# Kernel tuning notes

Measured on AMD Instinct MI355X. Metric: run time of the kernel, lower is better.

Reference implementation:

```python
import jax, jax.numpy as jnp
import numpy as np

EPS = 1e-5

def conv2d(x, w, b, stride, pad):
    out = jax.lax.conv_general_dilated(x, w, (stride, stride), [(pad, pad), (pad, pad)],
                                       dimension_numbers=('NCHW', 'OIHW', 'NCHW'))
    return out + b[None, :, None, None]

def instance_norm(x):
    # nn.InstanceNorm2d default: affine=False, eps=1e-5, per (N,C) over (H,W)
    m = jnp.mean(x, axis=(2, 3), keepdims=True)
    v = jnp.var(x, axis=(2, 3), keepdims=True)
    return (x - m) * jax.lax.rsqrt(v + EPS)

def deform_conv2d(x, offset, mask, w, b, stride, pad):
    # x: [N,Cin,H,W]; offset: [N,2K,Ho,Wo] as [dy(K);dx(K)]; mask: [N,K,Ho,Wo]
    N, Cin, H, W = x.shape
    Cout, _, kh, kw = w.shape
    K = kh * kw
    Ho, Wo = mask.shape[2], mask.shape[3]
    oy, ox = offset[:, :K], offset[:, K:]
    ky, kx = jnp.meshgrid(jnp.arange(kh), jnp.arange(kw), indexing='ij')
    ky = ky.reshape(K).astype(x.dtype)
    kx = kx.reshape(K).astype(x.dtype)
    base_y = (jnp.arange(Ho) * stride - pad).astype(x.dtype)
    base_x = (jnp.arange(Wo) * stride - pad).astype(x.dtype)
    # sampling coords [N,K,Ho,Wo]
    py = base_y[None, None, :, None] + ky[None, :, None, None] + oy
    px = base_x[None, None, None, :] + kx[None, :, None, None] + ox
    y0 = jnp.floor(py)
    x0 = jnp.floor(px)
    wy = (py - y0)[:, None]  # [N,1,K,Ho,Wo]
    wx = (px - x0)[:, None]
    flat = x.reshape(N, Cin, H * W)

    def sample(yi, xi):
        valid = ((yi >= 0) & (yi <= H - 1) & (xi >= 0) & (xi <= W - 1)).astype(x.dtype)
        yc = jnp.clip(yi, 0, H - 1).astype(jnp.int32)
        xc = jnp.clip(xi, 0, W - 1).astype(jnp.int32)
        idx = yc * W + xc  # [N,K,Ho,Wo]
        vals = jax.vmap(lambda f, i: f[:, i])(flat, idx)  # [N,Cin,K,Ho,Wo]
        return vals * valid[:, None]

    v00 = sample(y0, x0)
    v01 = sample(y0, x0 + 1)
    v10 = sample(y0 + 1, x0)
    v11 = sample(y0 + 1, x0 + 1)
    samp = (v00 * (1 - wy) * (1 - wx) + v01 * (1 - wy) * wx
            + v10 * wy * (1 - wx) + v11 * wy * wx)
    samp = samp * mask[:, None]  # modulated (DCNv2)
    out = jnp.einsum('nckhw,ock->nohw', samp, w.reshape(Cout, Cin, K))
    return out + b[None, :, None, None]

def mdcp(x, off_w, off_b, dcn_w, dcn_b, stride, pad):
    # ModulatedDeformConvPack.forward with input_offset == input_real == x
    o = conv2d(x, off_w, off_b, stride, pad)
    K = o.shape[1] // 3
    o1, o2, m = o[:, :K], o[:, K:2 * K], o[:, 2 * K:]
    offset = jnp.concatenate([o1, o2], axis=1)
    mask = jax.nn.sigmoid(m)
    return deform_conv2d(x, offset, mask, dcn_w, dcn_b, stride, pad)

def res_block(x, w1, b1, w2, b2):
    # MUNIT-style ResBlock: [reflect-pad conv3x3, IN, ReLU] -> [reflect-pad conv3x3, IN] + skip
    h = jnp.pad(x, ((0, 0), (0, 0), (1, 1), (1, 1)), mode='reflect')
    h = jax.nn.relu(instance_norm(conv2d(h, w1, b1, 1, 0)))
    h = jnp.pad(h, ((0, 0), (0, 0), (1, 1), (1, 1)), mode='reflect')
    h = instance_norm(conv2d(h, w2, b2, 1, 0))
    return x + h

def setup_inputs() -> dict:
    key = jax.random.key(0)
    ks = jax.random.split(key, 32)
    N, H, W = 2, 256, 256

    def wconv(k, shape, scale=None):
        if scale is None:
            scale = 1.0 / np.sqrt(shape[1] * shape[2] * shape[3])
        return jax.random.normal(k, shape, jnp.float32) * scale

    def bias(k, n, scale=0.01):
        return jax.random.normal(k, (n,), jnp.float32) * scale

    inp = {}
    inp['x'] = jax.random.normal(ks[0], (N, 3, H, W), jnp.float32)
    # offset/mask convs: small weights (sub-pixel offsets; trained-from-zero in original)
    inp['off1_w'] = wconv(ks[1], (147, 3, 7, 7), 0.01)
    inp['off1_b'] = bias(ks[2], 147)
    inp['dcn1_w'] = wconv(ks[3], (64, 3, 7, 7))
    inp['dcn1_b'] = bias(ks[4], 64)
    inp['off2_w'] = wconv(ks[5], (48, 64, 4, 4), 0.01)
    inp['off2_b'] = bias(ks[6], 48)
    inp['dcn2_w'] = wconv(ks[7], (128, 64, 4, 4))
    inp['dcn2_b'] = bias(ks[8], 128)
    inp['off3_w'] = wconv(ks[9], (48, 128, 4, 4), 0.01)
    inp['off3_b'] = bias(ks[10], 48)
    inp['dcn3_w'] = wconv(ks[11], (256, 128, 4, 4))
    inp['dcn3_b'] = bias(ks[12], 256)
    for i, base in ((1, 13), (2, 17)):
        inp[f'rb{i}_w1'] = wconv(ks[base], (256, 256, 3, 3))
        inp[f'rb{i}_b1'] = bias(ks[base + 1], 256)
        inp[f'rb{i}_w2'] = wconv(ks[base + 2], (256, 256, 3, 3))
        inp[f'rb{i}_b2'] = bias(ks[base + 3], 256)
    return inp

def reference(x, off1_w, off1_b, dcn1_w, dcn1_b, off2_w, off2_b, dcn2_w, dcn2_b,
              off3_w, off3_b, dcn3_w, dcn3_b,
              rb1_w1, rb1_b1, rb1_w2, rb1_b2, rb2_w1, rb2_b1, rb2_w2, rb2_b2):
    h = jax.nn.relu(instance_norm(mdcp(x, off1_w, off1_b, dcn1_w, dcn1_b, 1, 3)))
    skip1 = h
    h = jax.nn.relu(instance_norm(mdcp(h, off2_w, off2_b, dcn2_w, dcn2_b, 2, 1)))
    skip2 = h
    h = jax.nn.relu(instance_norm(mdcp(h, off3_w, off3_b, dcn3_w, dcn3_b, 2, 1)))
    h = res_block(h, rb1_w1, rb1_b1, rb1_w2, rb1_b2)
    h = res_block(h, rb2_w1, rb2_b1, rb2_w2, rb2_b2)
    return (h, skip1, skip2)
```

## Files before the change

kernel.cpp:

```cpp
#include <hip/hip_runtime.h>
#include <hip/hip_bf16.h>
#include <math.h>

#define TPB 256
typedef __hip_bfloat16 bf16;
typedef short bf16x8 __attribute__((ext_vector_type(8)));
typedef float f32x4 __attribute__((ext_vector_type(4)));

constexpr long BIASF  = 0;
constexpr long RB1W1T = 2048;
constexpr long RB1W2T = 591872;
constexpr long RB2W1T = 1181696;
constexpr long RB2W2T = 1771520;
constexpr long FB     = 2361344;
constexpr long WB1OT  = 2361344;
constexpr long WB1DT  = 2382956;
constexpr long WO2T   = 2392364;
constexpr long WB2T   = 2441516;
constexpr long WO3T   = 2572588;
constexpr long WB3T   = 2670892;
constexpr long OFFB   = 3221504;
constexpr long H3F    = 4458496;
constexpr long PSUM   = 5507072;
constexpr long PSQ    = 5515264;
constexpr long CLBUF  = 5523456;
constexpr long OFF1B = 0,   DCN1B = 147;
constexpr long OFF2B = 211, DCN2B = 259;
constexpr long OFF3B = 387, DCN3B = 435;
constexpr long RB1B1 = 691, RB1B2 = 947;
constexpr long RB2B1 = 1203, RB2B2 = 1459;

template<int BF>
__device__ __forceinline__ float ldT(const void* p, long i) {
    if (BF) {
        unsigned short h = ((const unsigned short*)p)[i];
        return __uint_as_float(((unsigned int)h) << 16);
    }
    return ((const float*)p)[i];
}
template<int BF>
__device__ __forceinline__ void stT(void* p, long i, float v) {
    if (BF) ((bf16*)p)[i] = __float2bfloat16(v);
    else    ((float*)p)[i] = v;
}
__device__ __forceinline__ float bitsToF(unsigned short h) {
    return __uint_as_float(((unsigned int)h) << 16);
}
__device__ __forceinline__ unsigned short fToBits(float v) {
    bf16 h = __float2bfloat16(v);
    return *(unsigned short*)&h;
}

__global__ void detect_kernel(const void* __restrict__ x, int* __restrict__ flag) {
    if (threadIdx.x == 0 && blockIdx.x == 0) {
        const unsigned short* u = (const unsigned short*)x;
        int sane = 0;
        for (int i = 0; i < 256; ++i) {
            float v = bitsToF(u[i]);
            float a = fabsf(v);
            if (a > 0.0009f && a < 1100.f) ++sane;
        }
        *flag = (sane >= 224) ? 1 : 0;
    }
}

struct PtrPack { const void* p[20]; };

template<int BF>
__device__ void repack_all_body(PtrPack pp, float* __restrict__ fw)
{
    constexpr int  bcum  [11] = {0,147,211,259,387,435,691,947,1203,1459,1715};
    int j0 = blockIdx.x * 1024 + threadIdx.x * 4;
    #pragma unroll
    for (int q = 0; q < 4; ++q) {
        int j = j0 + q;
        if (j < 1715) {
            int v = 0;
            #pragma unroll
            for (int s = 1; s < 10; ++s) if (j >= bcum[s]) v = s;
            fw[BIASF + j] = ldT<BF>(pp.p[10 + v], j - bcum[v]);
        }
    }
}
__global__ __launch_bounds__(TPB) void repack_all_kernel(
    PtrPack pp, float* fw, const int* dflag) {
    if (*dflag) repack_all_body<1>(pp, fw);
    else        repack_all_body<0>(pp, fw);
}

__global__ __launch_bounds__(TPB) void repack_dcn_kernel(
    const void* __restrict__ w2, const void* __restrict__ w3,
    const void* __restrict__ w1o, const void* __restrict__ w1d,
    const void* __restrict__ w2o, const void* __restrict__ w3o,
    float* __restrict__ fw, const int* __restrict__ dflag)
{
    int bf = *dflag;
    unsigned short* wb2 = (unsigned short*)(fw + WB2T);
    unsigned short* wb3 = (unsigned short*)(fw + WB3T);
    unsigned short* wb1o = (unsigned short*)(fw + WB1OT);
    unsigned short* wb1d = (unsigned short*)(fw + WB1DT);
    unsigned short* wb2o = (unsigned short*)(fw + WO2T);
    unsigned short* wb3o = (unsigned short*)(fw + WO3T);
    int b = blockIdx.x;
    if (b < 128) {
        int e0 = b * 1024 + threadIdx.x * 4;
        #pragma unroll
        for (int j = 0; j < 4; ++j) {
            int e = e0 + j;
            int co = e >> 10, rem = e & 1023, k = rem >> 6, ci = rem & 63;
            long si = ((long)(co * 64 + ci)) * 16 + k;
            float v = bf ? ldT<1>(w2, si) : ldT<0>(w2, si);
            wb2[e] = fToBits(v);
        }
    } else if (b < 640) {
        int e0 = (b - 128) * 1024 + threadIdx.x * 4;
        #pragma unroll
        for (int j = 0; j < 4; ++j) {
            int e = e0 + j;
            int co = e >> 11, rem = e & 2047, k = rem >> 7, ci = rem & 127;
            long si = ((long)(co * 128 + ci)) * 16 + k;
            float v = bf ? ldT<1>(w3, si) : ldT<0>(w3, si);
            wb3[e] = fToBits(v);
        }
    } else if (b < 665) {
        int e0 = (b - 640) * 1024 + threadIdx.x * 4;
        #pragma unroll
        for (int j = 0; j < 4; ++j) {
            int e = e0 + j;
            int co = e / 160, k = e - co * 160;
            float v = 0.f;
            if (co < 147 && k < 147) {
                long si = (long)co * 147 + k;
                v = bf ? ldT<1>(w1o, si) : ldT<0>(w1o, si);
            }
            wb1o[e] = fToBits(v);
        }
    } else if (b < 675) {
        int e0 = (b - 665) * 1024 + threadIdx.x * 4;
        #pragma unroll
        for (int j = 0; j < 4; ++j) {
            int e = e0 + j;
            int co = e / 160, k = e - co * 160;
            float v = 0.f;
            if (k < 147) {
                long si = (long)co * 147 + k;
                v = bf ? ldT<1>(w1d, si) : ldT<0>(w1d, si);
            }
            wb1d[e] = fToBits(v);
        }
    } else if (b < 739) {
        int e0 = (b - 675) * 1024 + threadIdx.x * 4;
        #pragma unroll
        for (int j = 0; j < 4; ++j) {
            int e = e0 + j;
            int co = e >> 10, rem = e & 1023, k = rem >> 6, ci = rem & 63;
            float v = 0.f;
            if (co < 48) {
                long si = ((long)(co * 64 + ci)) * 16 + k;
                v = bf ? ldT<1>(w2o, si) : ldT<0>(w2o, si);
            }
            wb2o[e] = fToBits(v);
        }
    } else {
        int e0 = (b - 739) * 1024 + threadIdx.x * 4;
        #pragma unroll
        for (int j = 0; j < 4; ++j) {
            int e = e0 + j;
            int co = e >> 11, rem = e & 2047, k = rem >> 7, ci = rem & 127;
            float v = 0.f;
            if (co < 48) {
                long si = ((long)(co * 128 + ci)) * 16 + k;
                v = bf ? ldT<1>(w3o, si) : ldT<0>(w3o, si);
            }
            wb3o[e] = fToBits(v);
        }
    }
}

struct RbPack { const void* src[4]; };
__global__ __launch_bounds__(TPB) void repack_rb_kernel(
    RbPack rp, float* fw, const int* dflag)
{
    __shared__ unsigned short lw[4 * 2304];
    int b = blockIdx.x;
    int ten = b >> 6;
    int co0 = (b & 63) * 4;
    const void* src = rp.src[ten];
    const long dstOff[4] = {RB1W1T, RB1W2T, RB2W1T, RB2W2T};
    unsigned short* dst = (unsigned short*)(fw + dstOff[ten]);
    int bf = *dflag;
    int t = threadIdx.x;
    for (int e = t; e < 4 * 2304; e += TPB) {
        int coL = e / 2304, i = e - coL * 2304;
        long si = (long)(co0 + coL) * 2304 + i;
        float v = bf ? ldT<1>(src, si) : ldT<0>(src, si);
        lw[e] = fToBits(v);
    }
    __syncthreads();
    for (int e = t; e < 9216; e += TPB) {
        int ci = e & 255, coL = (e >> 8) & 3, q = e >> 10;
        dst[((long)q * 256 + co0 + coL) * 256 + ci] = lw[coL * 2304 + ci * 9 + q];
    }
}

template<int BF>
__device__ void layer1_mfma_body(
    const void* __restrict__ x, const unsigned short* __restrict__ wo,
    const unsigned short* __restrict__ wd, const float* __restrict__ bias1,
    const float* __restrict__ bias2, void* __restrict__ out, long obase,
    float* xs, unsigned short* A, float* offs)
{
    int b = blockIdx.x;
    int n = b >> 11;
    int ho = (b >> 3) & 255;
    int wo0 = (b & 7) << 5;
    long xn = (long)n * 3 * 65536;
    int t = threadIdx.x;

    for (int e = t; e < 3 * 7 * 40; e += TPB) {
        int cc = e % 40; int rr = (e / 40) % 7; int ci = e / 280;
        int yy = ho - 3 + rr; int xx = wo0 - 3 + cc;
        float v = 0.f;
        if (cc < 38 && yy >= 0 && yy < 256 && xx >= 0 && xx < 256)
            v = ldT<BF>(x, xn + (long)ci * 65536 + yy * 256 + xx);
        xs[e] = v;
    }
    __syncthreads();

    for (int e = t; e < 5120; e += TPB) {
        int m = e & 31, k = e >> 5;
        float v = 0.f;
        if (k < 147) {
            int ci = k / 49, q = k - ci * 49;
            int ky = q / 7, kx = q - ky * 7;
            v = xs[(ci * 7 + ky) * 40 + m + kx];
        }
        A[(k >> 5) * 1024 + m * 32 + (k & 31)] = fToBits(v);
    }
    __syncthreads();

    int wv = t >> 6, lane = t & 63;
    int quad = lane >> 4, l16 = lane & 15;
    int mt = wv & 1, ntb = wv >> 1;

    {
        f32x4 acc[5];
        #pragma unroll
        for (int j = 0; j < 5; ++j) acc[j] = (f32x4){0.f, 0.f, 0.f, 0.f};
        #pragma unroll
        for (int kc = 0; kc < 5; ++kc) {
            bf16x8 a = *(const bf16x8*)&A[(kc * 32 + mt * 16 + l16) * 32 + quad * 8];
            #pragma unroll
            for (int j = 0; j < 5; ++j) {
                int ch = (ntb + 2 * j) * 16 + l16;
                bf16x8 bw = *(const bf16x8*)&wo[ch * 160 + kc * 32 + quad * 8];
                acc[j] = __builtin_amdgcn_mfma_f32_16x16x32_bf16(a, bw, acc[j], 0, 0, 0);
            }
        }
        #pragma unroll
        for (int j = 0; j < 5; ++j) {
            int ch = (ntb + 2 * j) * 16 + l16;
            if (ch < 147) {
                float bv = bias1[ch];
                #pragma unroll
                for (int reg = 0; reg < 4; ++reg) {
                    int m = mt * 16 + quad * 4 + reg;
                    offs[ch * 34 + m] = acc[j][reg] + bv;
                }
            }
        }
    }
    __syncthreads();

    for (int e = t; e < 49 * 32; e += TPB) {
        int p = e & 31; int k = e >> 5;
        float oy = offs[k * 34 + p];
        float ox = offs[(49 + k) * 34 + p];
        float mr = offs[(98 + k) * 34 + p];
        float m = 1.f / (1.f + expf(-mr));
        float py = (float)(ho - 3 + k / 7) + oy;
        float px = (float)(wo0 + p - 3 + k % 7) + ox;
        float y0f = floorf(py), x0f = floorf(px);
        float wy = py - y0f, wx = px - x0f;
        int y0 = (int)y0f, x0 = (int)x0f;
        bool yv0 = (y0 >= 0) && (y0 < 256);
        bool yv1 = (y0 + 1 >= 0) && (y0 + 1 < 256);
        bool xv0 = (x0 >= 0) && (x0 < 256);
        bool xv1 = (x0 + 1 >= 0) && (x0 + 1 < 256);
        int y0c = min(max(y0, 0), 255), y1c = min(max(y0 + 1, 0), 255);
        int x0c = min(max(x0, 0), 255), x1c = min(max(x0 + 1, 0), 255);
        float w00 = (yv0 && xv0) ? (1.f - wy) * (1.f - wx) * m : 0.f;
        float w01 = (yv0 && xv1) ? (1.f - wy) * wx * m : 0.f;
        float w10 = (yv1 && xv0) ? wy * (1.f - wx) * m : 0.f;
        float w11 = (yv1 && xv1) ? wy * wx * m : 0.f;
        #pragma unroll
        for (int ci = 0; ci < 3; ++ci) {
            long xc = xn + (long)ci * 65536;
            float v00 = ldT<BF>(x, xc + y0c * 256 + x0c);
            float v01 = ldT<BF>(x, xc + y0c * 256 + x1c);
            float v10 = ldT<BF>(x, xc + y1c * 256 + x0c);
            float v11 = ldT<BF>(x, xc + y1c * 256 + x1c);
            float val = w00 * v00 + w01 * v01 + w10 * v10 + w11 * v11;
            int k2 = ci * 49 + k;
            A[(k2 >> 5) * 1024 + p * 32 + (k2 & 31)] = fToBits(val);
        }
    }
    __syncthreads();

    f32x4 acc2[2];
    acc2[0] = (f32x4){0.f, 0.f, 0.f, 0.f};
    acc2[1] = (f32x4){0.f, 0.f, 0.f, 0.f};
    #pragma unroll
    for (int kc = 0; kc < 5; ++kc) {
        bf16x8 a = *(const bf16x8*)&A[(kc * 32 + mt * 16 + l16) * 32 + quad * 8];
        #pragma unroll
        for (int j = 0; j < 2; ++j) {
            int co = (ntb + 2 * j) * 16 + l16;
            bf16x8 bw = *(const bf16x8*)&wd[co * 160 + kc * 32 + quad * 8];
            acc2[j] = __builtin_amdgcn_mfma_f32_16x16x32_bf16(a, bw, acc2[j], 0, 0, 0);
        }
    }
    #pragma unroll
    for (int j = 0; j < 2; ++j) {
        int co = (ntb + 2 * j) * 16 + l16;
        float bv = bias2[co];
        #pragma unroll
        for (int reg = 0; reg < 4; ++reg) {
            int wox = wo0 + mt * 16 + quad * 4 + reg;
            long oi = obase + ((long)(n * 64 + co) * 256 + ho) * 256 + wox;
            stT<BF>(out, oi, acc2[j][reg] + bv);
        }
    }
}

__global__ __launch_bounds__(TPB) void layer1_mfma_kernel(
    const void* x, const unsigned short* wo, const unsigned short* wd,
    const float* bias1, const float* bias2, void* out, long obase, const int* dflag)
{
    __shared__ __align__(16) float xs[3 * 7 * 40];
    __shared__ __align__(16) unsigned short A[5120];
    __shared__ __align__(16) float offs[147 * 34];
    if (*dflag) layer1_mfma_body<1>(x, wo, wd, bias1, bias2, out, obase, xs, A, offs);
    else        layer1_mfma_body<0>(x, wo, wd, bias1, bias2, out, obase, xs, A, offs);
}

template<int CIN, int HH, int WW, int HO, int WO>
__global__ __launch_bounds__(TPB) void offconv_mfma_kernel(
    const unsigned short* __restrict__ xcl, const unsigned short* __restrict__ wb,
    const float* __restrict__ bias_f, float* __restrict__ out)
{
    constexpr int S   = 16 * CIN;
    constexpr int KL  = 512 / CIN;
    constexpr int NCH = 16 / KL;
    constexpr int PAIRS_W = (KL * 16) / 4;
    constexpr int TILES = (HO * WO) / 16;

    __shared__ int tp[256];
    __shared__ __align__(16) unsigned short smp[16 * 512];

    int tile = blockIdx.x % TILES;
    int n    = blockIdx.x / TILES;
    int lp0  = tile * 16;

    {
        int pr = threadIdx.x;
        int k = pr >> 4, p = pr & 15;
        int lp = lp0 + p;
        int ho = lp / WO, wo = lp - ho * WO;
        int yy = ho * 2 - 1 + (k >> 2);
        int xx = wo * 2 - 1 + (k & 3);
        bool valid = (yy >= 0) && (yy < HH) && (xx >= 0) && (xx < WW);
        tp[pr] = valid ? (yy * WW + xx) * CIN : -1;
    }

    int wv = threadIdx.x >> 6, lane = threadIdx.x & 63;
    int quad = lane >> 4, l16 = lane & 15;
    const unsigned short* xn = xcl + (long)n * HH * WW * CIN;

    f32x4 acc = (f32x4){0.f, 0.f, 0.f, 0.f};

    for (int ch = 0; ch < NCH; ++ch) {
        __syncthreads();
        #pragma unroll 4
        for (int u = 0; u < PAIRS_W; ++u) {
            int prl = wv * PAIRS_W + u;
            int pi  = ch * (KL * 16) + prl;
            int kl = prl >> 4, p = prl & 15;
            int t0 = tp[pi];
            #pragma unroll
            for (int cg = 0; cg < CIN / 64; ++cg) {
                int ci = cg * 64 + lane;
                unsigned short v = (t0 >= 0) ? xn[t0 + ci] : (unsigned short)0;
                int il = kl * CIN + ci;
                smp[((il >> 5) * 16 + p) * 32 + (il & 31)] = v;
            }
        }
        __syncthreads();
        #pragma unroll 4
        for (int kk = 0; kk < 16; ++kk) {
            bf16x8 a = *(const bf16x8*)&smp[(kk * 16 + l16) * 32 + quad * 8];
            int co = wv * 16 + l16;
            bf16x8 b = *(const bf16x8*)&wb[(long)co * S + ch * 512 + kk * 32 + quad * 8];
            acc = __builtin_amdgcn_mfma_f32_16x16x32_bf16(a, b, acc, 0, 0, 0);
        }
    }

    int co = wv * 16 + l16;
    if (co < 48) {
        float bv = bias_f[co];
        #pragma unroll
        for (int reg = 0; reg < 4; ++reg) {
            int lp = lp0 + quad * 4 + reg;
            int ho = lp / WO, wo = lp - ho * WO;
            out[((long)(n * 48 + co) * HO + ho) * WO + wo] = acc[reg] + bv;
        }
    }
}

template<int C>
__global__ __launch_bounds__(TPB) void nchw_to_cl_kernel(
    const void* __restrict__ in, long ibase, unsigned short* __restrict__ out,
    int HW, const int* __restrict__ dflag)
{
    __shared__ unsigned short tile[C * 65];
    int bf = *dflag;
    int n   = (blockIdx.x * 64) / HW;
    int px0 = (blockIdx.x * 64) % HW;
    for (int e = threadIdx.x; e < C * 64; e += TPB) {
        int c = e >> 6, p = e & 63;
        long si = ibase + (long)(n * C + c) * HW + px0 + p;
        float v = bf ? ldT<1>(in, si) : ldT<0>(in, si);
        tile[c * 65 + p] = fToBits(v);
    }
    __syncthreads();
    for (int e = threadIdx.x; e < C * 64; e += TPB) {
        int p = e / C, c = e - p * C;
        out[((long)n * HW + px0 + p) * C + c] = tile[c * 65 + p];
    }
}

template<int MODE, int CIN, int COUT, int CHALVES, int HH, int WW, int HO, int WO>
__global__ __launch_bounds__(TPB) void deform_mfma_kernel(
    const unsigned short* __restrict__ xcl, const float* __restrict__ off,
    const unsigned short* __restrict__ wb, const float* __restrict__ bias_f,
    void* __restrict__ outp, long obase, const int* __restrict__ dflag)
{
    constexpr int S   = 16 * CIN;
    constexpr int KL  = 512 / CIN;
    constexpr int NCH = 16 / KL;
    constexpr int PAIRS_W = (KL * 16) / 4;
    constexpr int TILES = (HO * WO) / 16;

    __shared__ int   tp[4][256];
    __shared__ float tw[4][256];
    __shared__ __align__(16) unsigned short smp[16 * 512];

    int half = (CHALVES == 1) ? 0 : (int)(blockIdx.x % CHALVES);
    int bb   = (CHALVES == 1) ? (int)blockIdx.x : (int)(blockIdx.x / CHALVES);
    int tile = bb % TILES;
    int n    = bb / TILES;
    int lp0  = tile * 16;

    {
        int pr = threadIdx.x;
        int k = pr >> 4, p = pr & 15;
        int lp = lp0 + p;
        int ho = lp / WO, wo = lp - ho * WO;
        long plane = (long)HO * WO;
        const float* offn = off + (long)n * 48 * plane;
        float oy = offn[(long)k * plane + lp];
        float ox = offn[(long)(16 + k) * plane + lp];
        float mr = offn[(long)(2 * 16 + k) * plane + lp];
        float m = 1.f / (1.f + expf(-mr));
        float py = (float)(ho * 2 - 1 + (k >> 2)) + oy;
        float px = (float)(wo * 2 - 1 + (k & 3)) + ox;
        float y0f = floorf(py), x0f = floorf(px);
        float wy = py - y0f, wx = px - x0f;
        int y0 = (int)y0f, x0 = (int)x0f;
        bool yv0 = (y0 >= 0) && (y0 < HH);
        bool yv1 = (y0 + 1 >= 0) && (y0 + 1 < HH);
        bool xv0 = (x0 >= 0) && (x0 < WW);
        bool xv1 = (x0 + 1 >= 0) && (x0 + 1 < WW);
        int y0c = min(max(y0, 0), HH - 1), y1c = min(max(y0 + 1, 0), HH - 1);
        int x0c = min(max(x0, 0), WW - 1), x1c = min(max(x0 + 1, 0), WW - 1);
        tp[0][pr] = (y0c * WW + x0c) * CIN;
        tp[1][pr] = (y0c * WW + x1c) * CIN;
        tp[2][pr] = (y1c * WW + x0c) * CIN;
        tp[3][pr] = (y1c * WW + x1c) * CIN;
        tw[0][pr] = (yv0 && xv0) ? (1.f - wy) * (1.f - wx) * m : 0.f;
        tw[1][pr] = (yv0 && xv1) ? (1.f - wy) * wx * m : 0.f;
        tw[2][pr] = (yv1 && xv0) ? wy * (1.f - wx) * m : 0.f;
        tw[3][pr] = (yv1 && xv1) ? wy * wx * m : 0.f;
    }

    int wv = threadIdx.x >> 6, lane = threadIdx.x & 63;
    int quad = lane >> 4, l16 = lane & 15;
    int cb = half * (COUT / CHALVES) + wv * 32;
    const unsigned short* xn = xcl + (long)n * HH * WW * CIN;

    f32x4 acc[2];
    acc[0] = (f32x4){0.f, 0.f, 0.f, 0.f};
    acc[1] = (f32x4){0.f, 0.f, 0.f, 0.f};

    for (int ch = 0; ch < NCH; ++ch) {
        __syncthreads();
        #pragma unroll 4
        for (int u = 0; u < PAIRS_W; ++u) {
            int prl = wv * PAIRS_W + u;
            int pi  = ch * (KL * 16) + prl;
            int kl = prl >> 4, p = prl & 15;
            int t0 = tp[0][pi], t1 = tp[1][pi], t2 = tp[2][pi], t3 = tp[3][pi];
            float w0 = tw[0][pi], w1 = tw[1][pi], w2 = tw[2][pi], w3 = tw[3][pi];
            #pragma unroll
            for (int cg = 0; cg < CIN / 64; ++cg) {
                int ci = cg * 64 + lane;
                float v = w0 * bitsToF(xn[t0 + ci]) + w1 * bitsToF(xn[t1 + ci])
                        + w2 * bitsToF(xn[t2 + ci]) + w3 * bitsToF(xn[t3 + ci]);
                int il = kl * CIN + ci;
                smp[((il >> 5) * 16 + p) * 32 + (il & 31)] = fToBits(v);
            }
        }
        __syncthreads();
        #pragma unroll 4
        for (int kk = 0; kk < 16; ++kk) {
            bf16x8 a = *(const bf16x8*)&smp[(kk * 16 + l16) * 32 + quad * 8];
            #pragma unroll
            for (int f = 0; f < 2; ++f) {
                int co = cb + f * 16 + l16;
                bf16x8 b = *(const bf16x8*)&wb[(long)co * S + ch * 512 + kk * 32 + quad * 8];
                acc[f] = __builtin_amdgcn_mfma_f32_16x16x32_bf16(a, b, acc[f], 0, 0, 0);
            }
        }
    }

    if (MODE == 1) {
        unsigned short* oCL = (unsigned short*)outp;
        #pragma unroll
        for (int f = 0; f < 2; ++f) {
            int co = cb + f * 16 + l16;
            float bv = bias_f[co];
            #pragma unroll
            for (int reg = 0; reg < 4; ++reg) {
                int lp = lp0 + quad * 4 + reg;
                oCL[((long)n * HO * WO + lp) * COUT + co] = fToBits(acc[f][reg] + bv);
            }
        }
    } else {
        int bf = *dflag;
        #pragma unroll
        for (int f = 0; f < 2; ++f) {
            int co = cb + f * 16 + l16;
            float bv = bias_f[co];
            #pragma unroll
            for (int reg = 0; reg < 4; ++reg) {
                int lp = lp0 + quad * 4 + reg;
                int ho = lp / WO, wo = lp - ho * WO;
                long oi = obase + ((long)(n * COUT + co) * HO + ho) * WO + wo;
                if (bf) stT<1>(outp, oi, acc[f][reg] + bv);
                else    stT<0>(outp, oi, acc[f][reg] + bv);
            }
        }
    }
}

__global__ __launch_bounds__(TPB) void resconv_mfma_kernel(
    const unsigned short* __restrict__ X, const unsigned short* __restrict__ W,
    const float* __restrict__ bias_f, bf16* __restrict__ Y)
{
    __shared__ __align__(16) unsigned short xs[3 * 66 * 64];
    int b = blockIdx.x;
    int coO = b & 7, r = (b >> 3) & 63, n = b >> 9;
    int t = threadIdx.x;
    int wv = t >> 6;
    int lane = t & 63;
    int quad = lane >> 4, l16 = lane & 15;
    int rows[3];
    rows[0] = (r == 0) ? 1 : r - 1;
    rows[1] = r;
    rows[2] = (r == 63) ? 62 : r + 1;

    f32x4 acc[2];
    acc[0] = (f32x4){0.f, 0.f, 0.f, 0.f};
    acc[1] = (f32x4){0.f, 0.f, 0.f, 0.f};

    long xbase = (long)n * 4096 * 256;

    for (int ci0 = 0; ci0 < 256; ci0 += 64) {
        __syncthreads();
        for (int e = t; e < 3 * 66 * 8; e += TPB) {
            int oct = e & 7;
            int col = (e >> 3) % 66;
            int ky  = e / (66 * 8);
            int gx = col - 1;
            gx = (gx < 0) ? 1 : ((gx > 63) ? 62 : gx);
            bf16x8 v = *(const bf16x8*)&X[xbase + ((long)rows[ky] * 64 + gx) * 256 + ci0 + oct * 8];
            int slot = oct ^ (col & 7);
            *(bf16x8*)&xs[((ky * 66 + col) << 6) + slot * 8] = v;
        }
        __syncthreads();
        #pragma unroll
        for (int q = 0; q < 9; ++q) {
            int ky = q / 3, kx = q % 3;
            int col = wv * 16 + l16 + kx;
            int base = (ky * 66 + col) << 6;
            #pragma unroll
            for (int kh = 0; kh < 2; ++kh) {
                int slot = (kh * 4 + quad) ^ (col & 7);
                bf16x8 a = *(const bf16x8*)&xs[base + slot * 8];
                #pragma unroll
                for (int ct = 0; ct < 2; ++ct) {
                    int co = coO * 32 + ct * 16 + l16;
                    bf16x8 bw = *(const bf16x8*)&W[((long)q * 256 + co) * 256 + ci0 + kh * 32 + quad * 8];
                    acc[ct] = __builtin_amdgcn_mfma_f32_16x16x32_bf16(a, bw, acc[ct], 0, 0, 0);
                }
            }
        }
    }

    long ybase = ((long)n * 4096 + (long)r * 64) * 256;
    #pragma unroll
    for (int ct = 0; ct < 2; ++ct) {
        int co = coO * 32 + ct * 16 + l16;
        float bv = bias_f[co];
        #pragma unroll
        for (int reg = 0; reg < 4; ++reg) {
            int px = wv * 16 + quad * 4 + reg;
            Y[ybase + (long)px * 256 + co] = __float2bfloat16(acc[ct][reg] + bv);
        }
    }
}

__global__ __launch_bounds__(TPB) void cl_stats_kernel(
    const unsigned short* __restrict__ X, float* __restrict__ psum, float* __restrict__ psq)
{
    int blk = blockIdx.x;
    int chunk = blk & 15, n = blk >> 4;
    int co = threadIdx.x;
    float s = 0.f, sq = 0.f;
    const unsigned short* p = X + ((long)n * 4096 + chunk * 256) * 256 + co;
    for (int i = 0; i < 256; ++i) {
        float v = bitsToF(p[(long)i * 256]);
        s += v; sq += v * v;
    }
    psum[(n * 16 + chunk) * 256 + co] = s;
    psq [(n * 16 + chunk) * 256 + co] = sq;
}

__device__ __forceinline__ void cl_load_stats(
    const float* psum, const float* psq, int n, float* mv, float* iv)
{
    int t = threadIdx.x;
    float s = 0.f, sq = 0.f;
    for (int c = 0; c < 16; ++c) {
        s  += psum[(n * 16 + c) * 256 + t];
        sq += psq [(n * 16 + c) * 256 + t];
    }
    float mean = s / 4096.f;
    mv[t] = mean;
    iv[t] = rsqrtf(sq / 4096.f - mean * mean + 1e-5f);
    __syncthreads();
}

__global__ __launch_bounds__(TPB) void cl_apply_kernel(
    unsigned short* __restrict__ X, const float* __restrict__ psum,
    const float* __restrict__ psq, int relu)
{
    __shared__ float mv[256], iv[256];
    int y = blockIdx.x & 63, n = blockIdx.x >> 6;
    cl_load_stats(psum, psq, n, mv, iv);
    unsigned short* row = X + ((long)n * 4096 + y * 64) * 256;
    for (int e = threadIdx.x; e < 64 * 256; e += TPB) {
        int co = e & 255;
        float v = (bitsToF(row[e]) - mv[co]) * iv[co];
        if (relu) v = fmaxf(v, 0.f);
        row[e] = fToBits(v);
    }
}

__global__ __launch_bounds__(TPB) void cl_apply_add_kernel(
    const unsigned short* __restrict__ T, unsigned short* __restrict__ H,
    const float* __restrict__ psum, const float* __restrict__ psq)
{
    __shared__ float mv[256], iv[256];
    int y = blockIdx.x & 63, n = blockIdx.x >> 6;
    cl_load_stats(psum, psq, n, mv, iv);
    long base = ((long)n * 4096 + y * 64) * 256;
    for (int e = threadIdx.x; e < 64 * 256; e += TPB) {
        int co = e & 255;
        float v = bitsToF(H[base + e]) + (bitsToF(T[base + e]) - mv[co]) * iv[co];
        H[base + e] = fToBits(v);
    }
}

__global__ __launch_bounds__(TPB) void cl_apply_final_kernel(
    const unsigned short* __restrict__ T, const unsigned short* __restrict__ H,
    void* __restrict__ outp, const float* __restrict__ psum,
    const float* __restrict__ psq, const int* __restrict__ dflag)
{
    __shared__ float mv[256], iv[256];
    int y = blockIdx.x & 63, n = blockIdx.x >> 6;
    cl_load_stats(psum, psq, n, mv, iv);
    int bf = *dflag;
    int x = threadIdx.x & 63, cg = threadIdx.x >> 6;
    for (int co = cg; co < 256; co += 4) {
        long cli = ((long)(n * 64 + y) * 64 + x) * 256 + co;
        float v = bitsToF(H[cli]) + (bitsToF(T[cli]) - mv[co]) * iv[co];
        long oi = (((long)(n * 256 + co)) * 64 + y) * 64 + x;
        if (bf) ((bf16*)outp)[oi] = __float2bfloat16(v);
        else    ((float*)outp)[oi] = v;
    }
}

__device__ __forceinline__ void reduce2(float& sum, float& sq, float* s1, float* s2)
{
    for (int off = 32; off; off >>= 1) {
        sum += __shfl_down(sum, off, 64);
        sq  += __shfl_down(sq,  off, 64);
    }
    int nw = blockDim.x >> 6;
    int wid = threadIdx.x >> 6;
    if ((threadIdx.x & 63) == 0) { s1[wid] = sum; s2[wid] = sq; }
    __syncthreads();
    sum = 0.f; sq = 0.f;
    for (int w = 0; w < nw; ++w) { sum += s1[w]; sq += s2[w]; }
}

__global__ void instnorm_kernel(
    void* __restrict__ buf, long base0, const int* __restrict__ dflag,
    int HW, int relu)
{
    __shared__ float s1[16], s2[16];
    int bf = *dflag;
    long base = base0 + (long)blockIdx.x * HW;
    float sum = 0.f, sq = 0.f;
    for (int i = threadIdx.x; i < HW; i += blockDim.x) {
        float v = bf ? bitsToF(((const unsigned short*)buf)[base + i])
                     : ((const float*)buf)[base + i];
        sum += v; sq += v * v;
    }
    reduce2(sum, sq, s1, s2);
    float mean = sum / HW;
    float inv = rsqrtf(sq / HW - mean * mean + 1e-5f);
    for (int i = threadIdx.x; i < HW; i += blockDim.x) {
        float v = bf ? bitsToF(((const unsigned short*)buf)[base + i])
                     : ((const float*)buf)[base + i];
        v = (v - mean) * inv;
        if (relu) v = fmaxf(v, 0.f);
        if (bf) ((bf16*)buf)[base + i] = __float2bfloat16(v);
        else    ((float*)buf)[base + i] = v;
    }
}

extern "C" void kernel_launch(void* const* d_in, const int* in_sizes, int n_in,
                              void* d_out, int out_size, void* d_ws, size_t ws_size,
                              hipStream_t stream) {
    const void* x = d_in[0];

    const long SKIP1 = 2097152;
    const long SKIP2 = 10485760;

    int* dflag = (int*)d_ws;
    float* fw = (float*)((char*)d_ws + 64);

    unsigned short* t1 = (unsigned short*)(fw + FB);
    unsigned short* t2 = (unsigned short*)(fw + FB + 1048576);
    unsigned short* h3 = (unsigned short*)(fw + H3F);
    float* offb = fw + OFFB;
    float* psum = fw + PSUM;
    float* psq  = fw + PSQ;
    unsigned short* clbuf = (unsigned short*)(fw + CLBUF);
    const unsigned short* wb1o = (const unsigned short*)(fw + WB1OT);
    const unsigned short* wb1d = (const unsigned short*)(fw + WB1DT);
    const unsigned short* wb2o = (const unsigned short*)(fw + WO2T);
    const unsigned short* wb3o = (const unsigned short*)(fw + WO3T);
    const unsigned short* wb2 = (const unsigned short*)(fw + WB2T);
    const unsigned short* wb3 = (const unsigned short*)(fw + WB3T);
    const unsigned short* rbw1 = (const unsigned short*)(fw + RB1W1T);
    const unsigned short* rbw2 = (const unsigned short*)(fw + RB1W2T);
    const unsigned short* rbw3 = (const unsigned short*)(fw + RB2W1T);
    const unsigned short* rbw4 = (const unsigned short*)(fw + RB2W2T);

    detect_kernel<<<1, 64, 0, stream>>>(x, dflag);

    PtrPack pp;
    for (int i = 0; i < 10; ++i) pp.p[i] = nullptr;
    pp.p[10] = d_in[2];  pp.p[11] = d_in[4];  pp.p[12] = d_in[6];  pp.p[13] = d_in[8];
    pp.p[14] = d_in[10]; pp.p[15] = d_in[12]; pp.p[16] = d_in[14]; pp.p[17] = d_in[16];
    pp.p[18] = d_in[18]; pp.p[19] = d_in[20];
    repack_all_kernel<<<2, TPB, 0, stream>>>(pp, fw, dflag);
    repack_dcn_kernel<<<867, TPB, 0, stream>>>(
        d_in[7], d_in[11], d_in[1], d_in[3], d_in[5], d_in[9], fw, dflag);
    RbPack rp;
    rp.src[0] = d_in[13]; rp.src[1] = d_in[15]; rp.src[2] = d_in[17]; rp.src[3] = d_in[19];
    repack_rb_kernel<<<256, TPB, 0, stream>>>(rp, fw, dflag);

    layer1_mfma_kernel<<<4096, TPB, 0, stream>>>(
        x, wb1o, wb1d, fw + OFF1B, fw + DCN1B, d_out, SKIP1, dflag);
    instnorm_kernel<<<128, 1024, 0, stream>>>(d_out, SKIP1, dflag, 65536, 1);
    nchw_to_cl_kernel<64><<<2048, TPB, 0, stream>>>(d_out, SKIP1, clbuf, 65536, dflag);

    offconv_mfma_kernel<64, 256, 256, 128, 128><<<2048, TPB, 0, stream>>>(
        clbuf, wb2o, fw + OFF2B, offb);
    deform_mfma_kernel<0, 64, 128, 1, 256, 256, 128, 128><<<2048, TPB, 0, stream>>>(
        clbuf, offb, wb2, fw + DCN2B, d_out, SKIP2, dflag);
    instnorm_kernel<<<256, 512, 0, stream>>>(d_out, SKIP2, dflag, 16384, 1);
    nchw_to_cl_kernel<128><<<512, TPB, 0, stream>>>(d_out, SKIP2, clbuf, 16384, dflag);

    offconv_mfma_kernel<128, 128, 128, 64, 64><<<512, TPB, 0, stream>>>(
        clbuf, wb3o, fw + OFF3B, offb);
    deform_mfma_kernel<1, 128, 256, 2, 128, 128, 64, 64><<<1024, TPB, 0, stream>>>(
        clbuf, offb, wb3, fw + DCN3B, h3, 0, dflag);
    cl_stats_kernel<<<32, TPB, 0, stream>>>(h3, psum, psq);
    cl_apply_kernel<<<128, TPB, 0, stream>>>(h3, psum, psq, 1);

    resconv_mfma_kernel<<<1024, TPB, 0, stream>>>(h3, rbw1, fw + RB1B1, (bf16*)t1);
    cl_stats_kernel<<<32, TPB, 0, stream>>>(t1, psum, psq);
    cl_apply_kernel<<<128, TPB, 0, stream>>>(t1, psum, psq, 1);
    resconv_mfma_kernel<<<1024, TPB, 0, stream>>>(t1, rbw2, fw + RB1B2, (bf16*)t2);
    cl_stats_kernel<<<32, TPB, 0, stream>>>(t2, psum, psq);
    cl_apply_add_kernel<<<128, TPB, 0, stream>>>(t2, h3, psum, psq);

    resconv_mfma_kernel<<<1024, TPB, 0, stream>>>(h3, rbw3, fw + RB2B1, (bf16*)t1);
    cl_stats_kernel<<<32, TPB, 0, stream>>>(t1, psum, psq);
    cl_apply_kernel<<<128, TPB, 0, stream>>>(t1, psum, psq, 1);
    resconv_mfma_kernel<<<1024, TPB, 0, stream>>>(t1, rbw4, fw + RB2B2, (bf16*)t2);
    cl_stats_kernel<<<32, TPB, 0, stream>>>(t2, psum, psq);
    cl_apply_final_kernel<<<128, TPB, 0, stream>>>(t2, h3, d_out, psum, psq, dflag);
}
```

Baseline: 965.5 us.

## Vectorize deform sampling to 2-channel loads and merge channel halves into one block

The bilinear sampling loop in the deformable conv kernel now has each thread gather two adjacent bf16 channels with 32-bit loads and write a packed pair to shared memory. The per-pair offsets and weights are packed into one 8-int shared row so they can be fetched with two 16-byte loads. For the layer-3 deform conv, the two output-channel halves that used to run in separate blocks now share one 512-thread block, so the sampled tile is built once instead of twice. The costs are fewer blocks (512 instead of 1024) and a larger block, which may lower occupancy.

```diff
diff --git a/kernel.cpp b/kernel.cpp
--- a/kernel.cpp
+++ b/kernel.cpp
@@ -439,30 +439,30 @@
     }
 }
 
-template<int MODE, int CIN, int COUT, int CHALVES, int HH, int WW, int HO, int WO>
-__global__ __launch_bounds__(TPB) void deform_mfma_kernel(
+template<int MODE, int CIN, int COUT, int NWAVES, int HH, int WW, int HO, int WO>
+__global__ __launch_bounds__(NWAVES * 64) void deform_mfma_kernel(
     const unsigned short* __restrict__ xcl, const float* __restrict__ off,
     const unsigned short* __restrict__ wb, const float* __restrict__ bias_f,
     void* __restrict__ outp, long obase, const int* __restrict__ dflag)
 {
-    constexpr int S   = 16 * CIN;
-    constexpr int KL  = 512 / CIN;
-    constexpr int NCH = 16 / KL;
-    constexpr int PAIRS_W = (KL * 16) / 4;
+    constexpr int TPBk = NWAVES * 64;
+    constexpr int S    = 16 * CIN;
+    constexpr int KL   = 512 / CIN;
+    constexpr int NCH  = 16 / KL;
+    constexpr int CH2  = CIN / 2;
+    constexpr int ITER = (KL * 16 * CH2) / TPBk;
     constexpr int TILES = (HO * WO) / 16;
 
-    __shared__ int   tp[4][256];
-    __shared__ float tw[4][256];
+    __shared__ __align__(16) int tpw[256][8];
     __shared__ __align__(16) unsigned short smp[16 * 512];
 
-    int half = (CHALVES == 1) ? 0 : (int)(blockIdx.x % CHALVES);
-    int bb   = (CHALVES == 1) ? (int)blockIdx.x : (int)(blockIdx.x / CHALVES);
-    int tile = bb % TILES;
-    int n    = bb / TILES;
+    int tile = blockIdx.x % TILES;
+    int n    = blockIdx.x / TILES;
     int lp0  = tile * 16;
-
-    {
-        int pr = threadIdx.x;
+    int tid  = threadIdx.x;
+
+    if (tid < 256) {
+        int pr = tid;
         int k = pr >> 4, p = pr & 15;
         int lp = lp0 + p;
         int ho = lp / WO, wo = lp - ho * WO;
@@ -470,7 +470,7 @@
         const float* offn = off + (long)n * 48 * plane;
         float oy = offn[(long)k * plane + lp];
         float ox = offn[(long)(16 + k) * plane + lp];
-        float mr = offn[(long)(2 * 16 + k) * plane + lp];
+        float mr = offn[(long)(32 + k) * plane + lp];
         float m = 1.f / (1.f + expf(-mr));
         float py = (float)(ho * 2 - 1 + (k >> 2)) + oy;
         float px = (float)(wo * 2 - 1 + (k & 3)) + ox;
@@ -483,19 +483,19 @@
         bool xv1 = (x0 + 1 >= 0) && (x0 + 1 < WW);
         int y0c = min(max(y0, 0), HH - 1), y1c = min(max(y0 + 1, 0), HH - 1);
         int x0c = min(max(x0, 0), WW - 1), x1c = min(max(x0 + 1, 0), WW - 1);
-        tp[0][pr] = (y0c * WW + x0c) * CIN;
-        tp[1][pr] = (y0c * WW + x1c) * CIN;
-        tp[2][pr] = (y1c * WW + x0c) * CIN;
-        tp[3][pr] = (y1c * WW + x1c) * CIN;
-        tw[0][pr] = (yv0 && xv0) ? (1.f - wy) * (1.f - wx) * m : 0.f;
-        tw[1][pr] = (yv0 && xv1) ? (1.f - wy) * wx * m : 0.f;
-        tw[2][pr] = (yv1 && xv0) ? wy * (1.f - wx) * m : 0.f;
-        tw[3][pr] = (yv1 && xv1) ? wy * wx * m : 0.f;
-    }
-
-    int wv = threadIdx.x >> 6, lane = threadIdx.x & 63;
+        tpw[pr][0] = (y0c * WW + x0c) * CIN;
+        tpw[pr][1] = (y0c * WW + x1c) * CIN;
+        tpw[pr][2] = (y1c * WW + x0c) * CIN;
+        tpw[pr][3] = (y1c * WW + x1c) * CIN;
+        tpw[pr][4] = __float_as_int((yv0 && xv0) ? (1.f - wy) * (1.f - wx) * m : 0.f);
+        tpw[pr][5] = __float_as_int((yv0 && xv1) ? (1.f - wy) * wx * m : 0.f);
+        tpw[pr][6] = __float_as_int((yv1 && xv0) ? wy * (1.f - wx) * m : 0.f);
+        tpw[pr][7] = __float_as_int((yv1 && xv1) ? wy * wx * m : 0.f);
+    }
+
+    int wv = tid >> 6, lane = tid & 63;
     int quad = lane >> 4, l16 = lane & 15;
-    int cb = half * (COUT / CHALVES) + wv * 32;
+    int cb = (wv & 3) * 32 + (wv >> 2) * (COUT / 2);
     const unsigned short* xn = xcl + (long)n * HH * WW * CIN;
 
     f32x4 acc[2];
@@ -505,20 +505,29 @@
     for (int ch = 0; ch < NCH; ++ch) {
         __syncthreads();
         #pragma unroll 4
-        for (int u = 0; u < PAIRS_W; ++u) {
-            int prl = wv * PAIRS_W + u;
+        for (int it = 0; it < ITER; ++it) {
+            int e   = it * TPBk + tid;
+            int prl = e / CH2;
+            int ci  = (e - prl * CH2) * 2;
             int pi  = ch * (KL * 16) + prl;
-            int kl = prl >> 4, p = prl & 15;
-            int t0 = tp[0][pi], t1 = tp[1][pi], t2 = tp[2][pi], t3 = tp[3][pi];
-            float w0 = tw[0][pi], w1 = tw[1][pi], w2 = tw[2][pi], w3 = tw[3][pi];
-            #pragma unroll
-            for (int cg = 0; cg < CIN / 64; ++cg) {
-                int ci = cg * 64 + lane;
-                float v = w0 * bitsToF(xn[t0 + ci]) + w1 * bitsToF(xn[t1 + ci])
-                        + w2 * bitsToF(xn[t2 + ci]) + w3 * bitsToF(xn[t3 + ci]);
-                int il = kl * CIN + ci;
-                smp[((il >> 5) * 16 + p) * 32 + (il & 31)] = fToBits(v);
-            }
+            const int4   tp4 = *(const int4*)&tpw[pi][0];
+            const float4 tw4 = *(const float4*)&tpw[pi][4];
+            unsigned v0 = *(const unsigned*)(xn + tp4.x + ci);
+            unsigned v1 = *(const unsigned*)(xn + tp4.y + ci);
+            unsigned v2 = *(const unsigned*)(xn + tp4.z + ci);
+            unsigned v3 = *(const unsigned*)(xn + tp4.w + ci);
+            float r0 = tw4.x * bitsToF((unsigned short)(v0 & 0xffff))
+                     + tw4.y * bitsToF((unsigned short)(v1 & 0xffff))
+                     + tw4.z * bitsToF((unsigned short)(v2 & 0xffff))
+                     + tw4.w * bitsToF((unsigned short)(v3 & 0xffff));
+            float r1 = tw4.x * bitsToF((unsigned short)(v0 >> 16))
+                     + tw4.y * bitsToF((unsigned short)(v1 >> 16))
+                     + tw4.z * bitsToF((unsigned short)(v2 >> 16))
+                     + tw4.w * bitsToF((unsigned short)(v3 >> 16));
+            unsigned ov = (unsigned)fToBits(r0) | ((unsigned)fToBits(r1) << 16);
+            int il = (prl >> 4) * CIN + ci;
+            int p  = prl & 15;
+            *(unsigned*)&smp[((il >> 5) * 16 + p) * 32 + (il & 31)] = ov;
         }
         __syncthreads();
         #pragma unroll 4
@@ -801,14 +810,14 @@
 
     offconv_mfma_kernel<64, 256, 256, 128, 128><<<2048, TPB, 0, stream>>>(
         clbuf, wb2o, fw + OFF2B, offb);
-    deform_mfma_kernel<0, 64, 128, 1, 256, 256, 128, 128><<<2048, TPB, 0, stream>>>(
+    deform_mfma_kernel<0, 64, 128, 4, 256, 256, 128, 128><<<2048, TPB, 0, stream>>>(
         clbuf, offb, wb2, fw + DCN2B, d_out, SKIP2, dflag);
     instnorm_kernel<<<256, 512, 0, stream>>>(d_out, SKIP2, dflag, 16384, 1);
     nchw_to_cl_kernel<128><<<512, TPB, 0, stream>>>(d_out, SKIP2, clbuf, 16384, dflag);
 
     offconv_mfma_kernel<128, 128, 128, 64, 64><<<512, TPB, 0, stream>>>(
         clbuf, wb3o, fw + OFF3B, offb);
-    deform_mfma_kernel<1, 128, 256, 2, 128, 128, 64, 64><<<1024, TPB, 0, stream>>>(
+    deform_mfma_kernel<1, 128, 256, 8, 128, 128, 64, 64><<<512, 512, 0, stream>>>(
         clbuf, offb, wb3, fw + DCN3B, h3, 0, dflag);
     cl_stats_kernel<<<32, TPB, 0, stream>>>(h3, psum, psq);
     cl_apply_kernel<<<128, TPB, 0, stream>>>(h3, psum, psq, 1);
```

Measured after the change: 926.4 us. 1.04x faster.
